# Performance work log

Measured on AMD Instinct MI355X. Metric: run time of the kernel, lower is better.

The kernel has to match this reference:

```python
import jax, jax.numpy as jnp
import numpy as np

N = 8192        # nodes
FEAT = 256      # in_out_features
R = 65536       # relation instances
IN_RELS = 64
OUT_RELS = 64
M = 1 << 20     # (edge, relation) triples flattened from rel_dict
NEG = -1e9


def setup_inputs() -> dict:
    key = jax.random.key(0)
    k1, k2, k3, k4, k5, k6 = jax.random.split(key, 6)
    x = jax.random.normal(k1, (N, FEAT), dtype=jnp.float32)
    rel = jax.random.normal(k2, (R, IN_RELS), dtype=jnp.float32)
    # Conv1d(in_rels, out_rels, k=1, bias=False) weight, squeezed to [out_rels, in_rels]
    W = jax.random.normal(k3, (OUT_RELS, IN_RELS), dtype=jnp.float32) / np.sqrt(IN_RELS)
    bias = jnp.zeros((FEAT,), dtype=jnp.float32)
    pair_src = jax.random.randint(k4, (M,), 0, N, dtype=jnp.int32)
    pair_dst = jax.random.randint(k5, (M,), 0, N, dtype=jnp.int32)
    pair_rel = jax.random.randint(k6, (M,), 0, R, dtype=jnp.int32)
    # adj acts as an additive mask: 0 on edges (and self-loops), large negative elsewhere
    adj = jnp.full((N, N), NEG, dtype=jnp.float32)
    adj = adj.at[pair_src, pair_dst].set(0.0)
    adj = adj.at[jnp.arange(N), jnp.arange(N)].set(0.0)
    return {"input": x, "rel": rel, "W": W, "bias": bias, "adj": adj,
            "pair_src": pair_src, "pair_dst": pair_dst, "pair_rel": pair_rel}


def reference(input, rel, W, bias, adj, pair_src, pair_dst, pair_rel):
    # Conv1d k=1 over [1, in_rels, R] == matmul; only output channel 0 is ever used.
    seq_fts_rel0 = rel @ W[0]                     # [R]
    vals = seq_fts_rel0[pair_rel]                 # [M] per (edge, relation) value
    n = adj.shape[0]
    # Per-pair max over its relation set; zeros init matches torch's zeros_like(adj)
    # (negatives clipped to 0 are equivalent after the subsequent ReLU).
    logits = jnp.zeros((n, n), dtype=vals.dtype).at[pair_src, pair_dst].max(vals)
    coefs = jax.nn.softmax(jax.nn.relu(logits) + adj, axis=1)   # [N, N]
    ret = coefs @ input + bias                    # [N, FEAT]
    return jax.nn.elu(ret)                        # concat=True branch
```

## Files before the change

kernel.cpp:

```cpp
#include <hip/hip_runtime.h>
#include <math.h>

#define N_NODES  8192
#define FEATDIM  256
#define RCOUNT   65536
#define IN_RELS  64
#define M_PAIRS  1048576
#define LCAP     256
#define HSIZE    512

#define OFF_SEQ    0
#define OFF_CURSOR 262144
#define OFF_ROWCNT 294912
#define OFF_JV     327680
#define OFF_JL     17104896
#define OFF_WL     25493504
#define WS_NEEDED  33882112

__global__ void zero_kernel(int* __restrict__ p) {
    int i = blockIdx.x * blockDim.x + threadIdx.x;
    if (i < N_NODES) p[i] = 0;
}

__global__ void seq_kernel(const float* __restrict__ rel,
                           const float* __restrict__ W,
                           float* __restrict__ seq) {
    int r = blockIdx.x * blockDim.x + threadIdx.x;
    if (r >= RCOUNT) return;
    const float4* rr = reinterpret_cast<const float4*>(rel + (size_t)r * IN_RELS);
    const float4* ww = reinterpret_cast<const float4*>(W);
    float acc = 0.f;
#pragma unroll
    for (int k = 0; k < IN_RELS / 4; ++k) {
        float4 a = rr[k];
        float4 w = ww[k];
        acc += a.x * w.x + a.y * w.y + a.z * w.z + a.w * w.w;
    }
    seq[r] = acc;
}

__global__ void scatter_direct_kernel(const int* __restrict__ src,
                                      const int* __restrict__ dst,
                                      const int* __restrict__ prel,
                                      const float* __restrict__ seq,
                                      int* __restrict__ cursor,
                                      int2* __restrict__ jv) {
    int p = blockIdx.x * blockDim.x + threadIdx.x;
    if (p >= M_PAIRS) return;
    int s = src[p];
    if (s < 0 || s >= N_NODES) return;
    int j = dst[p];
    if (j < 0 || j >= N_NODES) return;
    int r = prel[p];
    if (r < 0 || r >= RCOUNT) return;
    int pos = atomicAdd(&cursor[s], 1);
    if (pos < LCAP) {
        float v = fmaxf(seq[r], 0.f);
        jv[(size_t)s * LCAP + pos] = make_int2(j, __float_as_int(v));
    }
}

__launch_bounds__(256)
__global__ void attn_hash_kernel(const int2* __restrict__ jv,
                                 const int* __restrict__ cursor,
                                 int* __restrict__ jl,
                                 float* __restrict__ wl,
                                 int* __restrict__ rowcnt) {
    __shared__ int   hkey[HSIZE];
    __shared__ int   hval[HSIZE];
    __shared__ float red[256];
    __shared__ int   nout;

    const int i = blockIdx.x;
    const int t = threadIdx.x;

    hkey[t] = -1;          hval[t] = -1;
    hkey[t + 256] = -1;    hval[t + 256] = -1;
    if (t == 0) nout = 0;
    __syncthreads();

    int cnt = cursor[i];
    if (cnt < 0) cnt = 0;
    if (cnt > LCAP) cnt = LCAP;

    for (int e = t; e < cnt; e += 256) {
        int2 p = jv[(size_t)i * LCAP + e];
        int j = p.x;
        unsigned slot = ((unsigned)j * 2654435761u >> 16) & (HSIZE - 1);
        for (;;) {
            int k = atomicCAS(&hkey[slot], -1, j);
            if (k == -1 || k == j) break;
            slot = (slot + 1) & (HSIZE - 1);
        }
        atomicMax(&hval[slot], p.y);
    }
    if (t == 0) {
        int j = i;
        unsigned slot = ((unsigned)j * 2654435761u >> 16) & (HSIZE - 1);
        for (;;) {
            int k = atomicCAS(&hkey[slot], -1, j);
            if (k == -1 || k == j) break;
            slot = (slot + 1) & (HSIZE - 1);
        }
        atomicMax(&hval[slot], 0);
    }
    __syncthreads();

    float m = 0.f;
    {
        if (hkey[t] >= 0)       m = fmaxf(m, __int_as_float(hval[t]));
        if (hkey[t + 256] >= 0) m = fmaxf(m, __int_as_float(hval[t + 256]));
    }
    red[t] = m;
    __syncthreads();
    for (int s2 = 128; s2 > 0; s2 >>= 1) {
        if (t < s2) red[t] = fmaxf(red[t], red[t + s2]);
        __syncthreads();
    }
    m = red[0];
    __syncthreads();

    float z = 0.f;
    {
        if (hkey[t] >= 0)       z += expf(__int_as_float(hval[t]) - m);
        if (hkey[t + 256] >= 0) z += expf(__int_as_float(hval[t + 256]) - m);
    }
    red[t] = z;
    __syncthreads();
    for (int s2 = 128; s2 > 0; s2 >>= 1) {
        if (t < s2) red[t] += red[t + s2];
        __syncthreads();
    }
    const float invZ = 1.f / red[0];
    __syncthreads();

#pragma unroll
    for (int half = 0; half < 2; ++half) {
        int s = t + half * 256;
        int k = hkey[s];
        if (k >= 0) {
            int idx = atomicAdd(&nout, 1);
            jl[(size_t)i * LCAP + idx] = k;
            wl[(size_t)i * LCAP + idx] = expf(__int_as_float(hval[s]) - m) * invZ;
        }
    }
    __syncthreads();
    if (t == 0) rowcnt[i] = nout;
}

__launch_bounds__(64)
__global__ void spmm_kernel(const float* __restrict__ x,
                            const float* __restrict__ bias,
                            const int* __restrict__ jl,
                            const float* __restrict__ wl,
                            const int* __restrict__ rowcnt,
                            float* __restrict__ out) {
    __shared__ int   sj[LCAP];
    __shared__ float sw[LCAP];
    const int row = blockIdx.x;
    const int q   = blockIdx.y;
    const int t   = threadIdx.x;

    int cnt = rowcnt[row];
    if (cnt < 0) cnt = 0;
    if (cnt > LCAP) cnt = LCAP;
    for (int e = t; e < cnt; e += 64) {
        sj[e] = jl[(size_t)row * LCAP + e];
        sw[e] = wl[(size_t)row * LCAP + e];
    }
    __syncthreads();

    const float* xq = x + (size_t)q * 64 + t;
    float a0 = 0.f, a1 = 0.f, a2 = 0.f, a3 = 0.f;
    float a4 = 0.f, a5 = 0.f, a6 = 0.f, a7 = 0.f;
    int e = 0;
    for (; e + 8 <= cnt; e += 8) {
        a0 += sw[e + 0] * xq[(size_t)sj[e + 0] * FEATDIM];
        a1 += sw[e + 1] * xq[(size_t)sj[e + 1] * FEATDIM];
        a2 += sw[e + 2] * xq[(size_t)sj[e + 2] * FEATDIM];
        a3 += sw[e + 3] * xq[(size_t)sj[e + 3] * FEATDIM];
        a4 += sw[e + 4] * xq[(size_t)sj[e + 4] * FEATDIM];
        a5 += sw[e + 5] * xq[(size_t)sj[e + 5] * FEATDIM];
        a6 += sw[e + 6] * xq[(size_t)sj[e + 6] * FEATDIM];
        a7 += sw[e + 7] * xq[(size_t)sj[e + 7] * FEATDIM];
    }
    for (; e < cnt; ++e) a0 += sw[e] * xq[(size_t)sj[e] * FEATDIM];
    float v = ((a0 + a1) + (a2 + a3)) + ((a4 + a5) + (a6 + a7)) + bias[q * 64 + t];
    out[(size_t)row * FEATDIM + q * 64 + t] = v > 0.f ? v : expm1f(v);
}

extern "C" void kernel_launch(void* const* d_in, const int* in_sizes, int n_in,
                              void* d_out, int out_size, void* d_ws, size_t ws_size,
                              hipStream_t stream) {
    if (ws_size < (size_t)WS_NEEDED) return;
    if (out_size < N_NODES * FEATDIM) return;
    if (n_in < 8) return;

    const float* x        = (const float*)d_in[0];
    const float* rel      = (const float*)d_in[1];
    const float* W        = (const float*)d_in[2];
    const float* bias     = (const float*)d_in[3];
    const int*   pair_src = (const int*)d_in[5];
    const int*   pair_dst = (const int*)d_in[6];
    const int*   pair_rel = (const int*)d_in[7];
    float* out = (float*)d_out;

    char* ws = (char*)d_ws;
    float* seq    = (float*)(ws + OFF_SEQ);
    int*   cursor = (int*)(ws + OFF_CURSOR);
    int*   rowcnt = (int*)(ws + OFF_ROWCNT);
    int2*  jv     = (int2*)(ws + OFF_JV);
    int*   jl     = (int*)(ws + OFF_JL);
    float* wl     = (float*)(ws + OFF_WL);

    zero_kernel<<<N_NODES / 256, 256, 0, stream>>>(cursor);
    seq_kernel<<<RCOUNT / 256, 256, 0, stream>>>(rel, W, seq);
    scatter_direct_kernel<<<M_PAIRS / 256, 256, 0, stream>>>(pair_src, pair_dst,
                                                             pair_rel, seq, cursor, jv);
    attn_hash_kernel<<<N_NODES, 256, 0, stream>>>(jv, cursor, jl, wl, rowcnt);
    spmm_kernel<<<dim3(N_NODES, 4), 64, 0, stream>>>(x, bias, jl, wl, rowcnt, out);
}
```

Measured before the change: 443.3 us.

## Fold cursor zeroing into seq kernel, use wave shuffles, pack index/weight pairs

Removes the separate zero kernel by clearing the cursor array inside seq_kernel. The softmax max and sum reductions now use wavefront shuffles and a four-entry shared array instead of a tree reduction with many barriers, and the exp values are reused rather than recomputed. The neighbor indices and weights are stored interleaved as int2, so spmm loads one array instead of two. This saves a launch, several block barriers and some memory traffic, but the spmm kernel is dominated by gathers from x, so the overall gain is likely modest.

```diff
diff --git a/kernel.cpp b/kernel.cpp
--- a/kernel.cpp
+++ b/kernel.cpp
@@ -13,19 +13,15 @@
 #define OFF_CURSOR 262144
 #define OFF_ROWCNT 294912
 #define OFF_JV     327680
-#define OFF_JL     17104896
-#define OFF_WL     25493504
+#define OFF_JW     17104896
 #define WS_NEEDED  33882112
-
-__global__ void zero_kernel(int* __restrict__ p) {
-    int i = blockIdx.x * blockDim.x + threadIdx.x;
-    if (i < N_NODES) p[i] = 0;
-}
 
 __global__ void seq_kernel(const float* __restrict__ rel,
                            const float* __restrict__ W,
-                           float* __restrict__ seq) {
+                           float* __restrict__ seq,
+                           int* __restrict__ cursor) {
     int r = blockIdx.x * blockDim.x + threadIdx.x;
+    if (r < N_NODES) cursor[r] = 0;
     if (r >= RCOUNT) return;
     const float4* rr = reinterpret_cast<const float4*>(rel + (size_t)r * IN_RELS);
     const float4* ww = reinterpret_cast<const float4*>(W);
@@ -63,19 +59,21 @@
 __launch_bounds__(256)
 __global__ void attn_hash_kernel(const int2* __restrict__ jv,
                                  const int* __restrict__ cursor,
-                                 int* __restrict__ jl,
-                                 float* __restrict__ wl,
+                                 int2* __restrict__ jw,
                                  int* __restrict__ rowcnt) {
     __shared__ int   hkey[HSIZE];
     __shared__ int   hval[HSIZE];
-    __shared__ float red[256];
+    __shared__ float redm[4];
+    __shared__ float redz[4];
     __shared__ int   nout;
 
-    const int i = blockIdx.x;
-    const int t = threadIdx.x;
-
-    hkey[t] = -1;          hval[t] = -1;
-    hkey[t + 256] = -1;    hval[t + 256] = -1;
+    const int i    = blockIdx.x;
+    const int t    = threadIdx.x;
+    const int lane = t & 63;
+    const int wid  = t >> 6;
+
+    hkey[t] = -1;       hkey[t + 256] = -1;
+    hval[t] = -1;       hval[t + 256] = -1;
     if (t == 0) nout = 0;
     __syncthreads();
 
@@ -106,57 +104,48 @@
     }
     __syncthreads();
 
+    const int   k0 = hkey[t];
+    const int   k1 = hkey[t + 256];
+    const float v0 = __int_as_float(hval[t]);
+    const float v1 = __int_as_float(hval[t + 256]);
+
     float m = 0.f;
-    {
-        if (hkey[t] >= 0)       m = fmaxf(m, __int_as_float(hval[t]));
-        if (hkey[t + 256] >= 0) m = fmaxf(m, __int_as_float(hval[t + 256]));
-    }
-    red[t] = m;
-    __syncthreads();
-    for (int s2 = 128; s2 > 0; s2 >>= 1) {
-        if (t < s2) red[t] = fmaxf(red[t], red[t + s2]);
-        __syncthreads();
-    }
-    m = red[0];
-    __syncthreads();
-
-    float z = 0.f;
-    {
-        if (hkey[t] >= 0)       z += expf(__int_as_float(hval[t]) - m);
-        if (hkey[t + 256] >= 0) z += expf(__int_as_float(hval[t + 256]) - m);
-    }
-    red[t] = z;
-    __syncthreads();
-    for (int s2 = 128; s2 > 0; s2 >>= 1) {
-        if (t < s2) red[t] += red[t + s2];
-        __syncthreads();
-    }
-    const float invZ = 1.f / red[0];
-    __syncthreads();
-
+    if (k0 >= 0) m = fmaxf(m, v0);
+    if (k1 >= 0) m = fmaxf(m, v1);
 #pragma unroll
-    for (int half = 0; half < 2; ++half) {
-        int s = t + half * 256;
-        int k = hkey[s];
-        if (k >= 0) {
-            int idx = atomicAdd(&nout, 1);
-            jl[(size_t)i * LCAP + idx] = k;
-            wl[(size_t)i * LCAP + idx] = expf(__int_as_float(hval[s]) - m) * invZ;
-        }
-    }
-    __syncthreads();
-    if (t == 0) rowcnt[i] = nout;
+    for (int off = 32; off > 0; off >>= 1) m = fmaxf(m, __shfl_xor(m, off, 64));
+    if (lane == 0) redm[wid] = m;
+    __syncthreads();
+    m = fmaxf(fmaxf(redm[0], redm[1]), fmaxf(redm[2], redm[3]));
+
+    float e0 = 0.f, e1 = 0.f, z = 0.f;
+    if (k0 >= 0) { e0 = expf(v0 - m); z += e0; }
+    if (k1 >= 0) { e1 = expf(v1 - m); z += e1; }
+#pragma unroll
+    for (int off = 32; off > 0; off >>= 1) z += __shfl_xor(z, off, 64);
+    if (lane == 0) redz[wid] = z;
+    __syncthreads();
+    const float invZ = 1.f / (((redz[0] + redz[1]) + (redz[2] + redz[3])));
+
+    if (k0 >= 0) {
+        int idx = atomicAdd(&nout, 1);
+        if (idx < LCAP) jw[(size_t)i * LCAP + idx] = make_int2(k0, __float_as_int(e0 * invZ));
+    }
+    if (k1 >= 0) {
+        int idx = atomicAdd(&nout, 1);
+        if (idx < LCAP) jw[(size_t)i * LCAP + idx] = make_int2(k1, __float_as_int(e1 * invZ));
+    }
+    __syncthreads();
+    if (t == 0) rowcnt[i] = nout < LCAP ? nout : LCAP;
 }
 
 __launch_bounds__(64)
 __global__ void spmm_kernel(const float* __restrict__ x,
                             const float* __restrict__ bias,
-                            const int* __restrict__ jl,
-                            const float* __restrict__ wl,
+                            const int2* __restrict__ jw,
                             const int* __restrict__ rowcnt,
                             float* __restrict__ out) {
-    __shared__ int   sj[LCAP];
-    __shared__ float sw[LCAP];
+    __shared__ int2 s[LCAP];
     const int row = blockIdx.x;
     const int q   = blockIdx.y;
     const int t   = threadIdx.x;
@@ -164,10 +153,7 @@
     int cnt = rowcnt[row];
     if (cnt < 0) cnt = 0;
     if (cnt > LCAP) cnt = LCAP;
-    for (int e = t; e < cnt; e += 64) {
-        sj[e] = jl[(size_t)row * LCAP + e];
-        sw[e] = wl[(size_t)row * LCAP + e];
-    }
+    for (int e = t; e < cnt; e += 64) s[e] = jw[(size_t)row * LCAP + e];
     __syncthreads();
 
     const float* xq = x + (size_t)q * 64 + t;
@@ -175,16 +161,16 @@
     float a4 = 0.f, a5 = 0.f, a6 = 0.f, a7 = 0.f;
     int e = 0;
     for (; e + 8 <= cnt; e += 8) {
-        a0 += sw[e + 0] * xq[(size_t)sj[e + 0] * FEATDIM];
-        a1 += sw[e + 1] * xq[(size_t)sj[e + 1] * FEATDIM];
-        a2 += sw[e + 2] * xq[(size_t)sj[e + 2] * FEATDIM];
-        a3 += sw[e + 3] * xq[(size_t)sj[e + 3] * FEATDIM];
-        a4 += sw[e + 4] * xq[(size_t)sj[e + 4] * FEATDIM];
-        a5 += sw[e + 5] * xq[(size_t)sj[e + 5] * FEATDIM];
-        a6 += sw[e + 6] * xq[(size_t)sj[e + 6] * FEATDIM];
-        a7 += sw[e + 7] * xq[(size_t)sj[e + 7] * FEATDIM];
-    }
-    for (; e < cnt; ++e) a0 += sw[e] * xq[(size_t)sj[e] * FEATDIM];
+        a0 += __int_as_float(s[e + 0].y) * xq[(size_t)s[e + 0].x * FEATDIM];
+        a1 += __int_as_float(s[e + 1].y) * xq[(size_t)s[e + 1].x * FEATDIM];
+        a2 += __int_as_float(s[e + 2].y) * xq[(size_t)s[e + 2].x * FEATDIM];
+        a3 += __int_as_float(s[e + 3].y) * xq[(size_t)s[e + 3].x * FEATDIM];
+        a4 += __int_as_float(s[e + 4].y) * xq[(size_t)s[e + 4].x * FEATDIM];
+        a5 += __int_as_float(s[e + 5].y) * xq[(size_t)s[e + 5].x * FEATDIM];
+        a6 += __int_as_float(s[e + 6].y) * xq[(size_t)s[e + 6].x * FEATDIM];
+        a7 += __int_as_float(s[e + 7].y) * xq[(size_t)s[e + 7].x * FEATDIM];
+    }
+    for (; e < cnt; ++e) a0 += __int_as_float(s[e].y) * xq[(size_t)s[e].x * FEATDIM];
     float v = ((a0 + a1) + (a2 + a3)) + ((a4 + a5) + (a6 + a7)) + bias[q * 64 + t];
     out[(size_t)row * FEATDIM + q * 64 + t] = v > 0.f ? v : expm1f(v);
 }
@@ -210,13 +196,11 @@
     int*   cursor = (int*)(ws + OFF_CURSOR);
     int*   rowcnt = (int*)(ws + OFF_ROWCNT);
     int2*  jv     = (int2*)(ws + OFF_JV);
-    int*   jl     = (int*)(ws + OFF_JL);
-    float* wl     = (float*)(ws + OFF_WL);
-
-    zero_kernel<<<N_NODES / 256, 256, 0, stream>>>(cursor);
-    seq_kernel<<<RCOUNT / 256, 256, 0, stream>>>(rel, W, seq);
+    int2*  jw     = (int2*)(ws + OFF_JW);
+
+    seq_kernel<<<RCOUNT / 256, 256, 0, stream>>>(rel, W, seq, cursor);
     scatter_direct_kernel<<<M_PAIRS / 256, 256, 0, stream>>>(pair_src, pair_dst,
                                                              pair_rel, seq, cursor, jv);
-    attn_hash_kernel<<<N_NODES, 256, 0, stream>>>(jv, cursor, jl, wl, rowcnt);
-    spmm_kernel<<<dim3(N_NODES, 4), 64, 0, stream>>>(x, bias, jl, wl, rowcnt, out);
-}
+    attn_hash_kernel<<<N_NODES, 256, 0, stream>>>(jv, cursor, jw, rowcnt);
+    spmm_kernel<<<dim3(N_NODES, 4), 64, 0, stream>>>(x, bias, jw, rowcnt, out);
+}
```

Result: no change. 436.3 us (-1.6%).
